# Kernel tuning notes

Hardware: AMD Instinct MI355X
Metric: run time of the kernel (lower is better)

Reference implementation:

```python
import jax, jax.numpy as jnp
import numpy as np

B, L, D, H1, OUT, MAX_W = 16, 128, 768, 770, 40, 30


def _span_mask():
    # valid spans: i <= j and width < MAX_W (structured sparsity over the L x L grid)
    ii, jj = np.meshgrid(np.arange(L), np.arange(L), indexing='ij')
    return ((jj >= ii) & (jj - ii < MAX_W)).astype(np.int32)


def setup_inputs():
    key = jax.random.key(0)
    ks = jax.random.split(key, 5)
    hidden_states = jax.random.normal(ks[0], (B, L + 1, D), dtype=jnp.float32)
    rng = np.random.default_rng(0)
    starts = rng.integers(0, L - MAX_W, size=(B,))
    ends = starts + rng.integers(0, MAX_W, size=(B,))
    pred_spans = jnp.asarray(np.stack([starts, ends], axis=1), dtype=jnp.int32)
    span_mask = jnp.asarray(_span_mask())
    W1 = 0.02 * jax.random.normal(ks[1], (2 * D + 1, H1), dtype=jnp.float32)
    b1 = jax.random.normal(ks[2], (H1,), dtype=jnp.float32)
    W2 = 0.02 * jax.random.normal(ks[3], (H1, OUT), dtype=jnp.float32)
    b2 = jax.random.normal(ks[4], (OUT,), dtype=jnp.float32)
    return dict(hidden_states=hidden_states, pred_spans=pred_spans, token_num=L,
                span_available_indication_matrix=span_mask,
                W1=W1, b1=b1, W2=W2, b2=b2)


def reference(hidden_states, pred_spans, token_num, span_available_indication_matrix, W1, b1, W2, b2):
    # span mask is an integer constant -> resolve valid (i, j) pairs on host
    mask = np.asarray(span_available_indication_matrix)
    vi, vj = np.nonzero(mask == 1)            # [n_valid] each
    vi_j = jnp.asarray(vi)
    vj_j = jnp.asarray(vj)
    vecs = hidden_states[:, 1:token_num + 1, :]  # token t -> hidden[:, t+1, :], [B, L, D]
    xi = vecs[:, vi_j, :]                        # [B, n_valid, D] gather of span-start vecs
    xj = vecs[:, vj_j, :]                        # [B, n_valid, D] gather of span-end vecs
    # pred_indications: 2 if span == pred span; 1 if strictly inside it (i<=j); else 0
    s = pred_spans[:, 0:1]
    e = pred_spans[:, 1:2]
    i_ = vi_j[None, :]
    j_ = vj_j[None, :]
    exact = (i_ == s) & (j_ == e)
    inside = (i_ >= s) & (j_ <= e) & (i_ <= j_)
    ind = jnp.where(exact, 2.0, jnp.where(inside, 1.0, 0.0)).astype(hidden_states.dtype)  # [B, n_valid]
    # Linear over concat([xi, xj, ind]) expressed as split matmuls (avoids materializing concat)
    W1i, W1j, w1c = W1[:D], W1[D:2 * D], W1[2 * D]
    h = (jnp.einsum('bnd,dh->bnh', xi, W1i)
         + jnp.einsum('bnd,dh->bnh', xj, W1j)
         + ind[..., None] * w1c + b1)
    h = jax.nn.relu(h)
    logits = jnp.einsum('bnh,ho->bno', h, W2) + b2   # [B, n_valid, OUT]
    return jax.nn.log_softmax(logits, axis=-1)
```

## Files before the change

### kernel.cpp

```cpp
#include <hip/hip_runtime.h>
#include <math.h>

#define B_ 16
#define L_ 128
#define D_ 768
#define H1_ 770
#define OUT_ 40
#define NPAIRS 3405
#define NLOG 1540
#define YSB 1552
#define VOFFB 776
#define KPAD 800
#define W1TROWS 1600
#define NKS 25
#define NTILES 252
#define BSWZ_N (26 * 3 * 512)

#define NB_X 1536
#define NB_W 166
#define NB_T 1200
#define NB_A (NB_X + NB_W + NB_T)
#define NB_B 800
#define NB_C (63 * 8)

typedef __attribute__((ext_vector_type(8))) short bf16x8;
typedef __attribute__((ext_vector_type(8))) unsigned short u16x8;
typedef __attribute__((ext_vector_type(4))) float f32x4;
typedef __attribute__((ext_vector_type(2))) float f32x2;
typedef __attribute__((ext_vector_type(4))) unsigned int u32x4;

__device__ inline unsigned short f2bf(float f) {
  unsigned int u = __builtin_bit_cast(unsigned int, f);
  u += 0x7fffu + ((u >> 16) & 1u);
  return (unsigned short)(u >> 16);
}
__device__ inline float bf2f(unsigned short x) {
  return __builtin_bit_cast(float, (unsigned int)x << 16);
}
__device__ inline f32x2 unpk_bf(unsigned int d) {
  f32x2 r;
  r[0] = __builtin_bit_cast(float, d << 16);
  r[1] = __builtin_bit_cast(float, d & 0xffff0000u);
  return r;
}

#if __has_builtin(__builtin_amdgcn_cvt_pk_bf16_f32)
typedef __attribute__((ext_vector_type(2))) __bf16 bf16x2_t;
__device__ inline unsigned int pack_bf16(float lo, float hi) {
  bf16x2_t r = __builtin_amdgcn_cvt_pk_bf16_f32(lo, hi);
  return __builtin_bit_cast(unsigned int, r);
}
#else
__device__ inline unsigned int pack_bf16(float lo, float hi) {
  return (unsigned int)f2bf(lo) | ((unsigned int)f2bf(hi) << 16);
}
#endif

typedef const __attribute__((address_space(1))) void* gas_t;
typedef __attribute__((address_space(3))) void* las_t;
__device__ inline void gl2lds16(const void* g, void* l) {
  __builtin_amdgcn_global_load_lds((gas_t)g, (las_t)l, 16, 0, 0);
}

__device__ inline void tile_decode(int T, int& ti, int& d) {
  if (T < 216) { ti = T / 9; d = T - ti * 9; }
  else {
    int m = T - 216; int r = 24, w = 8;
    while (m >= w) { m -= w; --w; ++r; }
    ti = r; d = m;
  }
}
__device__ inline int pair_rank(int i, int j) {
  return (i < 99) ? i * 30 + (j - i)
                  : NPAIRS - (128 - i) * (129 - i) / 2 + (j - i);
}

__global__ __launch_bounds__(256) void prep_k(
    const float* __restrict__ hidden, const float* __restrict__ W1,
    const float* __restrict__ b1, const float* __restrict__ W2,
    unsigned short* __restrict__ Xb, unsigned short* __restrict__ W1T,
    unsigned short* __restrict__ Bswz, float* __restrict__ Cv)
{
  __shared__ float t[32][33];
  const int u = blockIdx.x;
  const int tid = threadIdx.x;

  if (u < NB_X) {
    int idx = u * 256 + tid;
    int m = idx / 192;
    int c = idx - m * 192;
    float4 f = *(const float4*)(hidden + (size_t)(m + (m >> 7) + 1) * D_ + c * 4);
    ushort4 o;
    o.x = f2bf(f.x); o.y = f2bf(f.y); o.z = f2bf(f.z); o.w = f2bf(f.w);
    *(ushort4*)(Xb + (size_t)m * D_ + c * 4) = o;
  } else if (u < NB_X + NB_W) {
    int idx = (u - NB_X) * 256 + tid;
    if (idx < BSWZ_N) {
      int ks = idx / 1536;
      int rem = idx - ks * 1536;
      int f = rem / 512;
      int l = (rem - f * 512) >> 3;
      int e = rem & 7;
      int n = f * 16 + (l & 15);
      int k = ks * 32 + (l >> 4) * 8 + e;
      float v = (n < OUT_ && k < H1_) ? W2[k * OUT_ + n] : 0.f;
      Bswz[idx] = f2bf(v);
    } else if (idx < BSWZ_N + 3 * KPAD) {
      int c = idx - BSWZ_N;
      int tt = c / KPAD, k = c - tt * KPAD;
      const float* w1c = W1 + 1536 * H1_;
      Cv[c] = (k < H1_) ? (b1[k] + (float)tt * w1c[k]) : 0.f;
    }
  } else {
    int bx = u - NB_X - NB_W;
    const int tx = tid & 31, ty = tid >> 5;
    const int n0 = (bx % 50) * 32, k0 = (bx / 50) * 32;
    #pragma unroll
    for (int r = 0; r < 4; ++r) {
      int k = k0 + ty + r * 8, n = n0 + tx;
      float v = 0.f;
      if (n < H1_)       v = W1[k * H1_ + n];
      else if (n < NLOG) v = W1[(D_ + k) * H1_ + (n - H1_)];
      t[ty + r * 8][tx] = v;
    }
    __syncthreads();
    #pragma unroll
    for (int r = 0; r < 4; ++r) {
      int n = n0 + ty + r * 8, k = k0 + tx;
      W1T[(size_t)n * D_ + k] = f2bf(t[tx][ty + r * 8]);
    }
  }
}

__global__ __launch_bounds__(256) void gemm_k(
    const unsigned short* __restrict__ Xb, const unsigned short* __restrict__ W1T,
    unsigned short* __restrict__ Yb)
{
  __shared__ unsigned short As[64][64];
  __shared__ unsigned short Bs[64][64];
  const int tid = threadIdx.x;
  const int lane = tid & 63, w = tid >> 6;
  const int lm = lane & 15, q = lane >> 4;
  const int xcd = blockIdx.x & 7;
  const int t = blockIdx.x >> 3;
  const int col0 = (t % 25) * 64;
  const int row0 = (xcd * 4 + t / 25) * 64;
  const int m0 = (w >> 1) * 32, n0 = (w & 1) * 32;

  const int srow = w * 16 + (lane >> 3);
  const int schunk = (((lane & 7) ^ ((lane >> 3) & 7))) * 8;
  const unsigned short* ga = Xb  + (size_t)(row0 + srow) * D_ + schunk;
  const unsigned short* gb = W1T + (size_t)(col0 + srow) * D_ + schunk;

  const int xs = lm & 7;

  f32x4 acc[2][2] = {};

  for (int k0 = 0; k0 < D_; k0 += 64) {
    gl2lds16(ga + k0,          &As[w * 16][0]);
    gl2lds16(ga + k0 + 8 * D_, &As[w * 16 + 8][0]);
    gl2lds16(gb + k0,          &Bs[w * 16][0]);
    gl2lds16(gb + k0 + 8 * D_, &Bs[w * 16 + 8][0]);
    __syncthreads();
    #pragma unroll
    for (int ks = 0; ks < 2; ++ks) {
      const int cc = ((ks * 4 + q) ^ xs) * 8;
      bf16x8 a0 = *(const bf16x8*)&As[m0 + lm]     [cc];
      bf16x8 a1 = *(const bf16x8*)&As[m0 + 16 + lm][cc];
      bf16x8 b0 = *(const bf16x8*)&Bs[n0 + lm]     [cc];
      bf16x8 b1 = *(const bf16x8*)&Bs[n0 + 16 + lm][cc];
      acc[0][0] = __builtin_amdgcn_mfma_f32_16x16x32_bf16(a0, b0, acc[0][0], 0, 0, 0);
      acc[0][1] = __builtin_amdgcn_mfma_f32_16x16x32_bf16(a0, b1, acc[0][1], 0, 0, 0);
      acc[1][0] = __builtin_amdgcn_mfma_f32_16x16x32_bf16(a1, b0, acc[1][0], 0, 0, 0);
      acc[1][1] = __builtin_amdgcn_mfma_f32_16x16x32_bf16(a1, b1, acc[1][1], 0, 0, 0);
    }
    __syncthreads();
  }

  #pragma unroll
  for (int ti = 0; ti < 2; ++ti) {
    #pragma unroll
    for (int tj = 0; tj < 2; ++tj) {
      int col = col0 + n0 + tj * 16 + lm;
      if (col >= NLOG) continue;
      int pc = (col < H1_) ? col : col + (VOFFB - H1_);
      #pragma unroll
      for (int r = 0; r < 4; ++r) {
        int row = row0 + m0 + ti * 16 + q * 4 + r;
        Yb[(size_t)row * YSB + pc] = f2bf(acc[ti][tj][r]);
      }
    }
  }
}

__global__ __launch_bounds__(512) void pair_k(
    const unsigned short* __restrict__ Yb, const int* __restrict__ spans,
    const unsigned short* __restrict__ Bswz, const float* __restrict__ Cv,
    const float* __restrict__ b2, float* __restrict__ out)
{
  __shared__ unsigned short Blds[NKS * 3 * 512];
  const int tid = threadIdx.x;
  const int w = tid >> 6;
  const int lane = tid & 63;
  const int u = blockIdx.x;
  const int bb = ((u & 7) << 1) | (w >> 2);
  const int T = (u >> 3) * 4 + (w & 3);
  const int lm = lane & 15, q = lane >> 4;

  for (int c = w; c < NKS * 3; c += 8)
    gl2lds16(Bswz + (size_t)c * 512 + lane * 8, &Blds[c * 512]);

  int ti, d;
  tile_decode(T, ti, d);
  const int i0 = ti * 4, j0 = (ti + d) * 4;

  const int ai = i0 + (lm & 3);
  const int aj = j0 + (lm >> 2);
  const int s = spans[2 * bb], e = spans[2 * bb + 1];
  const int ind = (ai == s && aj == e) ? 2 : ((ai >= s && aj <= e) ? 1 : 0);

  const unsigned short* uptr = Yb + (size_t)(bb * L_ + ai) * YSB + q * 8;
  const unsigned short* vptr = Yb + (size_t)(bb * L_ + aj) * YSB + VOFFB + q * 8;
  const float* cptr = Cv + ind * KPAD + q * 8;
  const unsigned short* bbase = Blds + lane * 8;

  __syncthreads();

  f32x4 acc0 = {}, acc1 = {}, acc2 = {};

  u16x8 uu0 = *(const u16x8*)(uptr);
  u16x8 vv0 = *(const u16x8*)(vptr);
  u16x8 uu1 = *(const u16x8*)(uptr + 32);
  u16x8 vv1 = *(const u16x8*)(vptr + 32);

  #pragma unroll 5
  for (int ks = 0; ks < NKS; ++ks) {
    const int ko = ks * 32;
    u16x8 cu = uu0, cw = vv0;
    uu0 = uu1; vv0 = vv1;
    uu1 = *(const u16x8*)(uptr + ko + 64);
    vv1 = *(const u16x8*)(vptr + ko + 64);
    bf16x8 b0  = *(const bf16x8*)(bbase + (size_t)(ks * 3 + 0) * 512);
    bf16x8 b1v = *(const bf16x8*)(bbase + (size_t)(ks * 3 + 1) * 512);
    bf16x8 b2f = *(const bf16x8*)(bbase + (size_t)(ks * 3 + 2) * 512);
    float4 c0 = *(const float4*)(cptr + ko);
    float4 c1 = *(const float4*)(cptr + ko + 4);
    u32x4 cud = __builtin_bit_cast(u32x4, cu);
    u32x4 cwd = __builtin_bit_cast(u32x4, cw);
    f32x2 cc01; cc01[0] = c0.x; cc01[1] = c0.y;
    f32x2 cc23; cc23[0] = c0.z; cc23[1] = c0.w;
    f32x2 cc45; cc45[0] = c1.x; cc45[1] = c1.y;
    f32x2 cc67; cc67[0] = c1.z; cc67[1] = c1.w;
    f32x2 zz = {};
    f32x2 h01 = __builtin_elementwise_max(unpk_bf(cud[0]) + unpk_bf(cwd[0]) + cc01, zz);
    f32x2 h23 = __builtin_elementwise_max(unpk_bf(cud[1]) + unpk_bf(cwd[1]) + cc23, zz);
    f32x2 h45 = __builtin_elementwise_max(unpk_bf(cud[2]) + unpk_bf(cwd[2]) + cc45, zz);
    f32x2 h67 = __builtin_elementwise_max(unpk_bf(cud[3]) + unpk_bf(cwd[3]) + cc67, zz);
    u32x4 hp;
    hp[0] = pack_bf16(h01[0], h01[1]);
    hp[1] = pack_bf16(h23[0], h23[1]);
    hp[2] = pack_bf16(h45[0], h45[1]);
    hp[3] = pack_bf16(h67[0], h67[1]);
    bf16x8 a = __builtin_bit_cast(bf16x8, hp);
    acc0 = __builtin_amdgcn_mfma_f32_16x16x32_bf16(a, b0, acc0, 0, 0, 0);
    acc1 = __builtin_amdgcn_mfma_f32_16x16x32_bf16(a, b1v, acc1, 0, 0, 0);
    acc2 = __builtin_amdgcn_mfma_f32_16x16x32_bf16(a, b2f, acc2, 0, 0, 0);
  }

  const float b2v0 = b2[lm];
  const float b2v1 = b2[16 + lm];
  const float b2v2 = (lm < 8) ? b2[32 + lm] : 0.f;

  #pragma unroll
  for (int r = 0; r < 4; ++r) {
    float l0 = acc0[r] + b2v0;
    float l1 = acc1[r] + b2v1;
    float l2 = (lm < 8) ? (acc2[r] + b2v2) : -INFINITY;
    float mx = fmaxf(fmaxf(l0, l1), l2);
    mx = fmaxf(mx, __shfl_xor(mx, 1));
    mx = fmaxf(mx, __shfl_xor(mx, 2));
    mx = fmaxf(mx, __shfl_xor(mx, 4));
    mx = fmaxf(mx, __shfl_xor(mx, 8));
    float sm = expf(l0 - mx) + expf(l1 - mx) + ((lm < 8) ? expf(l2 - mx) : 0.f);
    sm += __shfl_xor(sm, 1);
    sm += __shfl_xor(sm, 2);
    sm += __shfl_xor(sm, 4);
    sm += __shfl_xor(sm, 8);
    float lsd = mx + logf(sm);

    int pi_ = i0 + r, pj_ = j0 + q;
    if (pj_ >= pi_ && (pj_ - pi_) < 30) {
      float* op = out + ((size_t)bb * NPAIRS + pair_rank(pi_, pj_)) * OUT_;
      op[lm]      = l0 - lsd;
      op[16 + lm] = l1 - lsd;
      if (lm < 8) op[32 + lm] = l2 - lsd;
    }
  }
}

extern "C" void kernel_launch(void* const* d_in, const int* in_sizes, int n_in,
                              void* d_out, int out_size, void* d_ws, size_t ws_size,
                              hipStream_t stream) {
  const float* hidden = (const float*)d_in[0];
  const int*   spans  = (const int*)d_in[1];
  const float* W1 = (const float*)d_in[4];
  const float* b1 = (const float*)d_in[5];
  const float* W2 = (const float*)d_in[6];
  const float* b2 = (const float*)d_in[7];
  float* out = (float*)d_out;

  char* base = (char*)d_ws;
  size_t off = 0;
  auto take = [&](size_t bytes) {
    char* p = base + off;
    off = (off + bytes + 255) & ~(size_t)255;
    return p;
  };
  unsigned short* Yb   = (unsigned short*)take((size_t)2049 * YSB * 2);
  unsigned short* Xb   = (unsigned short*)take((size_t)2048 * D_ * 2);
  unsigned short* W1T  = (unsigned short*)take((size_t)W1TROWS * D_ * 2);
  unsigned short* Bswz = (unsigned short*)take((size_t)BSWZ_N * 2);
  float*          Cv   = (float*)take((size_t)3 * KPAD * 4);

  prep_k<<<dim3(NB_A), 256, 0, stream>>>(hidden, W1, b1, W2, Xb, W1T, Bswz, Cv);
  gemm_k<<<dim3(NB_B), 256, 0, stream>>>(Xb, W1T, Yb);
  pair_k<<<dim3(NB_C), 512, 0, stream>>>(Yb, spans, Bswz, Cv, b2, out);
}
```

Baseline: 114.0 us.

## Enlarge GEMM tiles to 128x128 with double-buffered LDS staging

Raises the GEMM block tile from 64x64 to 128x128, so each wave computes a 64x64 sub-tile with 16 MFMA accumulators. This cuts the block count from 800 to 208 and increases operand reuse per LDS load. LDS staging becomes double-buffered: the next k-slice is issued before computing the current one, and only one barrier remains per iteration. W1T padding and the transpose grid grow to 1664 rows so the 128-wide column tiles stay in bounds. In exchange, 208 blocks may underfill the 256 CUs, and the larger register and LDS footprint lowers occupancy.

```diff
diff --git a/kernel.cpp b/kernel.cpp
--- a/kernel.cpp
+++ b/kernel.cpp
@@ -11,16 +11,16 @@
 #define YSB 1552
 #define VOFFB 776
 #define KPAD 800
-#define W1TROWS 1600
+#define W1TROWS 1664
 #define NKS 25
 #define NTILES 252
 #define BSWZ_N (26 * 3 * 512)
 
 #define NB_X 1536
 #define NB_W 166
-#define NB_T 1200
+#define NB_T 1248
 #define NB_A (NB_X + NB_W + NB_T)
-#define NB_B 800
+#define NB_B 208
 #define NB_C (63 * 8)
 
 typedef __attribute__((ext_vector_type(8))) short bf16x8;
@@ -114,7 +114,7 @@
   } else {
     int bx = u - NB_X - NB_W;
     const int tx = tid & 31, ty = tid >> 5;
-    const int n0 = (bx % 50) * 32, k0 = (bx / 50) * 32;
+    const int n0 = (bx % 52) * 32, k0 = (bx / 52) * 32;
     #pragma unroll
     for (int r = 0; r < 4; ++r) {
       int k = k0 + ty + r * 8, n = n0 + tx;
@@ -136,54 +136,64 @@
     const unsigned short* __restrict__ Xb, const unsigned short* __restrict__ W1T,
     unsigned short* __restrict__ Yb)
 {
-  __shared__ unsigned short As[64][64];
-  __shared__ unsigned short Bs[64][64];
+  __shared__ unsigned short As[2][128][64];
+  __shared__ unsigned short Bs[2][128][64];
   const int tid = threadIdx.x;
   const int lane = tid & 63, w = tid >> 6;
   const int lm = lane & 15, q = lane >> 4;
-  const int xcd = blockIdx.x & 7;
-  const int t = blockIdx.x >> 3;
-  const int col0 = (t % 25) * 64;
-  const int row0 = (xcd * 4 + t / 25) * 64;
-  const int m0 = (w >> 1) * 32, n0 = (w & 1) * 32;
-
-  const int srow = w * 16 + (lane >> 3);
-  const int schunk = (((lane & 7) ^ ((lane >> 3) & 7))) * 8;
+  const int gt = (blockIdx.x & 7) * 26 + (blockIdx.x >> 3);
+  const int bm = gt / 13, bn = gt - bm * 13;
+  const int row0 = bm * 128, col0 = bn * 128;
+  const int m0 = (w >> 1) * 64, n0 = (w & 1) * 64;
+
+  const int srow = w * 32 + (lane >> 3);
+  const int schunk = ((lane & 7) ^ ((lane >> 3) & 7)) * 8;
   const unsigned short* ga = Xb  + (size_t)(row0 + srow) * D_ + schunk;
   const unsigned short* gb = W1T + (size_t)(col0 + srow) * D_ + schunk;
 
-  const int xs = lm & 7;
-
-  f32x4 acc[2][2] = {};
-
-  for (int k0 = 0; k0 < D_; k0 += 64) {
-    gl2lds16(ga + k0,          &As[w * 16][0]);
-    gl2lds16(ga + k0 + 8 * D_, &As[w * 16 + 8][0]);
-    gl2lds16(gb + k0,          &Bs[w * 16][0]);
-    gl2lds16(gb + k0 + 8 * D_, &Bs[w * 16 + 8][0]);
+  const int xk = lane & 7;
+
+  f32x4 acc[4][4] = {};
+
+  auto stage = [&](int bf, int k0) {
+    #pragma unroll
+    for (int i = 0; i < 4; ++i) {
+      gl2lds16(ga + k0 + (size_t)(8 * i) * D_, &As[bf][w * 32 + 8 * i][0]);
+      gl2lds16(gb + k0 + (size_t)(8 * i) * D_, &Bs[bf][w * 32 + 8 * i][0]);
+    }
+  };
+
+  stage(0, 0);
+  __syncthreads();
+
+  for (int t = 0; t < 12; ++t) {
+    if (t < 11) stage((t + 1) & 1, (t + 1) * 64);
+    const int bf = t & 1;
+    #pragma unroll
+    for (int ks = 0; ks < 2; ++ks) {
+      const int cc = ((ks * 4 + q) ^ xk) * 8;
+      bf16x8 av[4], bv[4];
+      #pragma unroll
+      for (int i = 0; i < 4; ++i) {
+        av[i] = *(const bf16x8*)&As[bf][m0 + 16 * i + lm][cc];
+        bv[i] = *(const bf16x8*)&Bs[bf][n0 + 16 * i + lm][cc];
+      }
+      #pragma unroll
+      for (int i = 0; i < 4; ++i)
+        #pragma unroll
+        for (int j = 0; j < 4; ++j)
+          acc[i][j] = __builtin_amdgcn_mfma_f32_16x16x32_bf16(av[i], bv[j], acc[i][j], 0, 0, 0);
+    }
     __syncthreads();
-    #pragma unroll
-    for (int ks = 0; ks < 2; ++ks) {
-      const int cc = ((ks * 4 + q) ^ xs) * 8;
-      bf16x8 a0 = *(const bf16x8*)&As[m0 + lm]     [cc];
-      bf16x8 a1 = *(const bf16x8*)&As[m0 + 16 + lm][cc];
-      bf16x8 b0 = *(const bf16x8*)&Bs[n0 + lm]     [cc];
-      bf16x8 b1 = *(const bf16x8*)&Bs[n0 + 16 + lm][cc];
-      acc[0][0] = __builtin_amdgcn_mfma_f32_16x16x32_bf16(a0, b0, acc[0][0], 0, 0, 0);
-      acc[0][1] = __builtin_amdgcn_mfma_f32_16x16x32_bf16(a0, b1, acc[0][1], 0, 0, 0);
-      acc[1][0] = __builtin_amdgcn_mfma_f32_16x16x32_bf16(a1, b0, acc[1][0], 0, 0, 0);
-      acc[1][1] = __builtin_amdgcn_mfma_f32_16x16x32_bf16(a1, b1, acc[1][1], 0, 0, 0);
-    }
-    __syncthreads();
   }
 
   #pragma unroll
-  for (int ti = 0; ti < 2; ++ti) {
-    #pragma unroll
-    for (int tj = 0; tj < 2; ++tj) {
-      int col = col0 + n0 + tj * 16 + lm;
-      if (col >= NLOG) continue;
-      int pc = (col < H1_) ? col : col + (VOFFB - H1_);
+  for (int tj = 0; tj < 4; ++tj) {
+    int col = col0 + n0 + tj * 16 + lm;
+    if (col >= NLOG) continue;
+    int pc = (col < H1_) ? col : col + (VOFFB - H1_);
+    #pragma unroll
+    for (int ti = 0; ti < 4; ++ti) {
       #pragma unroll
       for (int r = 0; r < 4; ++r) {
         int row = row0 + m0 + ti * 16 + q * 4 + r;
```

Result: slower. 120.9 us (+6.0%).
